# Kernel tuning notes

Hardware: AMD Instinct MI355X
Metric: run time of the kernel (lower is better)

The kernel has to match this reference:

```python
import jax, jax.numpy as jnp
import numpy as np

def setup_inputs() -> dict:
    key = jax.random.key(0)
    k1, k2 = jax.random.split(key)
    pcs1 = jax.random.normal(k1, (8, 4096, 3), dtype=jnp.float32)
    pcs2 = jax.random.normal(k2, (8, 4096, 3), dtype=jnp.float32)
    return {"pcs1": pcs1, "pcs2": pcs2}

def reference(pcs1, pcs2):
    # Pairwise squared L2 distances: [B, N, M]
    # ||a-b||^2 = ||a||^2 + ||b||^2 - 2 a.b
    sq1 = jnp.sum(pcs1 * pcs1, axis=-1)                # [B, N]
    sq2 = jnp.sum(pcs2 * pcs2, axis=-1)                # [B, M]
    inner = jnp.einsum('bnd,bmd->bnm', pcs1, pcs2)     # [B, N, M]
    d = sq1[:, :, None] + sq2[:, None, :] - 2.0 * inner
    d = jnp.maximum(d, 0.0)  # guard tiny negatives from cancellation
    dist1 = jnp.min(d, axis=2)   # [B, N] nearest in pcs2 for each point of pcs1
    dist2 = jnp.min(d, axis=1)   # [B, M] nearest in pcs1 for each point of pcs2
    loss1 = jnp.mean(jnp.sqrt(dist1))
    loss2 = jnp.mean(jnp.sqrt(dist2))
    return (loss1 + loss2) * 0.5
```

## Files before the change

### kernel.cpp

```cpp
#include <hip/hip_runtime.h>
#include <math.h>


typedef __attribute__((ext_vector_type(8)))  short bf16x8;
typedef __attribute__((ext_vector_type(16))) float f32x16;
typedef float f32x2 __attribute__((ext_vector_type(2)));

#define NPTS 4096
#define BATCH 8
#define NBLK_WORK 1024

union FragCast { uint4 u; bf16x8 v; };

__device__ __forceinline__ unsigned short f2bf(float f) {
    unsigned u = __float_as_uint(f);
    return (unsigned short)((u + 0x7FFFu + ((u >> 16) & 1u)) >> 16);
}
__device__ __forceinline__ float bf2f(unsigned short h) {
    return __uint_as_float(((unsigned)h) << 16);
}
__device__ __forceinline__ unsigned pk(unsigned short a, unsigned short b) {
    return (unsigned)a | ((unsigned)b << 16);
}

__device__ __forceinline__ void build_afrag(float x, float y, float z,
                                            uint4& a0, uint4& a1) {
    float sq  = fmaf(x, x, fmaf(y, y, z * z));
    float m2x = -2.0f * x, m2y = -2.0f * y, m2z = -2.0f * z;
    unsigned short hx = f2bf(m2x), hy = f2bf(m2y), hz = f2bf(m2z);
    unsigned short lx = f2bf(m2x - bf2f(hx));
    unsigned short ly = f2bf(m2y - bf2f(hy));
    unsigned short lz = f2bf(m2z - bf2f(hz));
    unsigned short sh = f2bf(sq);
    unsigned short sl = f2bf(sq - bf2f(sh));
    const unsigned short ONE = 0x3F80;
    a0 = make_uint4(pk(hx, hy), pk(hz, hx), pk(hy, hz), pk(lx, ly));
    a1 = make_uint4(pk(lz, lx), pk(ly, lz), pk(sh, sl), pk(ONE, ONE));
}

__device__ __forceinline__ uint4 build_bfrag(float x, float y, float z, int hf) {
    float sq = fmaf(x, x, fmaf(y, y, z * z));
    unsigned short px = f2bf(x), py = f2bf(y), pz = f2bf(z);
    unsigned short qx = f2bf(x - bf2f(px));
    unsigned short qy = f2bf(y - bf2f(py));
    unsigned short qz = f2bf(z - bf2f(pz));
    unsigned short sh = f2bf(sq);
    unsigned short sl = f2bf(sq - bf2f(sh));
    const unsigned short ONE = 0x3F80;
    return hf == 0
        ? make_uint4(pk(px, py), pk(pz, qx), pk(qy, qz), pk(px, py))
        : make_uint4(pk(pz, qx), pk(qy, qz), pk(ONE, ONE), pk(sh, sl));
}

__global__ __launch_bounds__(256, 4) void chamfer_fused(
    const float* __restrict__ pcs1, const float* __restrict__ pcs2,
    float* __restrict__ cpart, unsigned* __restrict__ counter)
{
    __shared__ uint4 afrag[2048];

    const int bid = blockIdx.x;
    const int dir = bid >> 9;
    const int b   = (bid >> 6) & 7;
    const int rq  = (bid >> 4) & 3;
    const int mg  = bid & 15;
    const int tid = threadIdx.x;

    if (bid == 0 && tid == 0) *counter = 0u;

    const float* bbase = (dir ? pcs2 : pcs1) + (size_t)b * NPTS * 3;
    const float* abase = (dir ? pcs1 : pcs2) + (size_t)b * NPTS * 3;

    const int w   = tid >> 6;
    const int l   = tid & 63;
    const int hf  = l >> 5;
    const int ln  = l & 31;

    {
        const float4* src = (const float4*)(abase + (size_t)rq * 3072);
        float4 f0 = src[3 * tid + 0];
        float4 f1 = src[3 * tid + 1];
        float4 f2 = src[3 * tid + 2];
        float xs[4] = {f0.x, f0.w, f1.z, f2.y};
        float ys[4] = {f0.y, f1.x, f1.w, f2.z};
        float zs[4] = {f0.z, f1.y, f2.x, f2.w};
        const int jt = tid >> 3;
        const int r0 = (tid & 7) * 4;
#pragma unroll
        for (int i = 0; i < 4; ++i) {
            uint4 a0, a1;
            build_afrag(xs[i], ys[i], zs[i], a0, a1);
            afrag[jt * 64 + r0 + i]      = a0;
            afrag[jt * 64 + 32 + r0 + i] = a1;
        }
    }
    __syncthreads();

    const f32x16 cz = {0.f,0.f,0.f,0.f,0.f,0.f,0.f,0.f,
                       0.f,0.f,0.f,0.f,0.f,0.f,0.f,0.f};

#pragma unroll 1
    for (int p = 0; p < 2; ++p) {
        const int mt = mg * 8 + w * 2 + p;

        FragCast bq;
        {
            const float* s = bbase + (size_t)(mt * 32 + ln) * 3;
            bq.u = build_bfrag(s[0], s[1], s[2], hf);
        }

        float acc[16];
#pragma unroll
        for (int i = 0; i < 16; ++i) acc[i] = 3.4e38f;

#pragma unroll 2
        for (int j = 0; j < 32; ++j) {
            FragCast aq;
            aq.u = afrag[j * 64 + hf * 32 + ln];
            f32x16 D = __builtin_amdgcn_mfma_f32_32x32x16_bf16(
                aq.v, bq.v, cz, 0, 0, 0);
#pragma unroll
            for (int i = 0; i < 16; ++i) acc[i] = fminf(acc[i], D[i]);
        }

        float m0 = fminf(acc[0],  acc[1]);
        float m1 = fminf(acc[2],  acc[3]);
        float m2 = fminf(acc[4],  acc[5]);
        float m3 = fminf(acc[6],  acc[7]);
        float m4 = fminf(acc[8],  acc[9]);
        float m5 = fminf(acc[10], acc[11]);
        float m6 = fminf(acc[12], acc[13]);
        float m7 = fminf(acc[14], acc[15]);
        float r  = fminf(fminf(fminf(m0, m1), fminf(m2, m3)),
                         fminf(fminf(m4, m5), fminf(m6, m7)));
        r = fminf(r, __shfl_xor(r, 32, 64));

        if (l < 32) {
            cpart[((((size_t)(dir * 8 + b) * 128 + mt) * 4 + rq) << 5) + ln] =
                fmaxf(r, 0.0f);
        }
    }
}

__global__ __launch_bounds__(256) void chamfer_red1(
    const float* __restrict__ cpart, float* __restrict__ bpart,
    unsigned* __restrict__ counter, float* __restrict__ out)
{
    __shared__ float ws4[4];
    __shared__ int islast;
    const int t  = threadIdx.x;
    const int tg = blockIdx.x * 256 + t;
    const float* p = cpart + ((size_t)(tg >> 5) << 7) + (tg & 31);
    float m = fminf(fminf(p[0], p[32]), fminf(p[64], p[96]));
    float s = sqrtf(m);
#pragma unroll
    for (int off = 1; off < 64; off <<= 1) s += __shfl_xor(s, off, 64);
    if ((t & 63) == 0) ws4[t >> 6] = s;
    __syncthreads();
    if (t == 0) {
        bpart[blockIdx.x] = ws4[0] + ws4[1] + ws4[2] + ws4[3];
        __threadfence();
        islast = (atomicAdd(counter, 1u) == 255u);
    }
    __syncthreads();
    if (islast) {
        __threadfence();
        float v = bpart[t];
#pragma unroll
        for (int off = 1; off < 64; off <<= 1) v += __shfl_xor(v, off, 64);
        if ((t & 63) == 0) ws4[t >> 6] = v;
        __syncthreads();
        if (t == 0)
            out[0] = (ws4[0] + ws4[1] + ws4[2] + ws4[3]) * (1.0f / 65536.0f);
    }
}

#define CPAIRS 1024
#define PA 16
#define RSTRIDE 68

__device__ __forceinline__ f32x2 pk_fma_lo(f32x2 c, f32x2 q, f32x2 acc) {
    f32x2 d;
    asm("v_pk_fma_f32 %0, %1, %2, %3 op_sel:[0,0,0] op_sel_hi:[0,1,1]"
        : "=v"(d) : "v"(c), "v"(q), "v"(acc));
    return d;
}
__device__ __forceinline__ f32x2 pk_fma_hi(f32x2 c, f32x2 q, f32x2 acc) {
    f32x2 d;
    asm("v_pk_fma_f32 %0, %1, %2, %3 op_sel:[1,0,0] op_sel_hi:[1,1,1]"
        : "=v"(d) : "v"(c), "v"(q), "v"(acc));
    return d;
}
__device__ __forceinline__ void vmin3(float& acc, float a, float b) {
    asm("v_min3_f32 %0, %1, %2, %3" : "=v"(acc) : "v"(acc), "v"(a), "v"(b));
}

__global__ __launch_bounds__(256, 4) void chamfer_vec(
    const float* __restrict__ pcs1, const float* __restrict__ pcs2,
    float* __restrict__ partials)
{
    __shared__ float4 lds[2 * CPAIRS];
    float4* bx = lds;
    float4* bz = lds + CPAIRS;

    const int bid = blockIdx.x;
    const int dir = bid >> 9;
    const int b   = (bid >> 6) & 7;
    const int ach = bid & 63;

    const float* A  = dir ? pcs2 : pcs1;
    const float* Bp = dir ? pcs1 : pcs2;
    const float* abase = A  + (size_t)b * NPTS * 3;
    const float* bbase = Bp + (size_t)b * NPTS * 3;

    const int tid = threadIdx.x;
    const int w   = tid >> 6;
    const int l   = tid & 63;

    const int apt = ach * 64 + w * PA;
    f32x2 cx[PA / 2], cy[PA / 2], cz2[PA / 2];
    float tmin[PA];
#pragma unroll
    for (int p2 = 0; p2 < PA / 2; ++p2) {
        const float* s = abase + (size_t)(apt + 2 * p2) * 3;
        cx[p2]  = (f32x2){-2.0f * s[0], -2.0f * s[3]};
        cy[p2]  = (f32x2){-2.0f * s[1], -2.0f * s[4]};
        cz2[p2] = (f32x2){-2.0f * s[2], -2.0f * s[5]};
        tmin[2 * p2] = 3.4e38f; tmin[2 * p2 + 1] = 3.4e38f;
    }

    for (int c = 0; c < 2; ++c) {
        if (c) __syncthreads();
#pragma unroll
        for (int i = 0; i < CPAIRS / 256; ++i) {
            int j  = i * 256 + tid;
            const float* s = bbase + (size_t)(c * CPAIRS + j) * 6;
            float x0 = s[0], y0 = s[1], z0 = s[2];
            float x1 = s[3], y1 = s[4], z1 = s[5];
            bx[j] = make_float4(x0, x1, y0, y1);
            bz[j] = make_float4(z0, z1,
                                fmaf(x0, x0, fmaf(y0, y0, z0 * z0)),
                                fmaf(x1, x1, fmaf(y1, y1, z1 * z1)));
        }
        __syncthreads();
#pragma unroll 4
        for (int t = 0; t < CPAIRS / 64; ++t) {
            float4 X = bx[t * 64 + l];
            float4 Z = bz[t * 64 + l];
            f32x2 qx = (f32x2){X.x, X.y};
            f32x2 qy = (f32x2){X.z, X.w};
            f32x2 qz = (f32x2){Z.x, Z.y};
            f32x2 qw = (f32x2){Z.z, Z.w};
#pragma unroll
            for (int p2 = 0; p2 < PA / 2; ++p2) {
                f32x2 d0 = pk_fma_lo(cz2[p2], qz, qw);
                d0 = pk_fma_lo(cy[p2], qy, d0);
                d0 = pk_fma_lo(cx[p2], qx, d0);
                vmin3(tmin[2 * p2], d0.x, d0.y);
                f32x2 d1 = pk_fma_hi(cz2[p2], qz, qw);
                d1 = pk_fma_hi(cy[p2], qy, d1);
                d1 = pk_fma_hi(cx[p2], qx, d1);
                vmin3(tmin[2 * p2 + 1], d1.x, d1.y);
            }
        }
    }

    __syncthreads();
    float* lds2 = (float*)lds;
#pragma unroll
    for (int p = 0; p < PA; ++p)
        lds2[(w * PA + p) * RSTRIDE + l] = tmin[p];
    __syncthreads();

    if (tid < 64) {
        const int g = tid;
        float m = 3.4e38f;
        const float4* row = (const float4*)&lds2[g * RSTRIDE];
#pragma unroll
        for (int i = 0; i < 16; ++i) {
            float4 v = row[i];
            m = fminf(fminf(m, fminf(v.x, v.y)), fminf(v.z, v.w));
        }
        const int ap = ach * 64 + g;
        float x = abase[ap * 3 + 0], y = abase[ap * 3 + 1], z = abase[ap * 3 + 2];
        float s = sqrtf(fmaxf(fmaf(x, x, fmaf(y, y, z * z)) + m, 0.0f));
#pragma unroll
        for (int off = 1; off < 64; off <<= 1) s += __shfl_xor(s, off, 64);
        if (g == 0) partials[bid] = s;
    }
}

__global__ __launch_bounds__(256) void chamfer_final(
    const float* __restrict__ partials, int n, float scale,
    float* __restrict__ out)
{
    __shared__ float ws4[4];
    const int t = threadIdx.x;
    float v = 0.0f;
    for (int i = t; i < n; i += 256) v += partials[i];
#pragma unroll
    for (int off = 1; off < 64; off <<= 1) v += __shfl_xor(v, off, 64);
    if ((t & 63) == 0) ws4[t >> 6] = v;
    __syncthreads();
    if (t == 0)
        out[0] = (ws4[0] + ws4[1] + ws4[2] + ws4[3]) * scale;
}

extern "C" void kernel_launch(void* const* d_in, const int* in_sizes, int n_in,
                              void* d_out, int out_size, void* d_ws, size_t ws_size,
                              hipStream_t stream) {
    const float* pcs1 = (const float*)d_in[0];
    const float* pcs2 = (const float*)d_in[1];
    float* out = (float*)d_out;

    const size_t MB = 1048576;
    const size_t need = MB + 4096;

    if (ws_size >= need) {
        char* w = (char*)d_ws;
        float*    cpart   = (float*)(w);
        float*    bpart   = (float*)(w + MB);
        unsigned* counter = (unsigned*)(w + MB + 1024);

        chamfer_fused<<<dim3(NBLK_WORK), dim3(256), 0, stream>>>(
            pcs1, pcs2, cpart, counter);
        chamfer_red1 <<<dim3(256), dim3(256), 0, stream>>>(
            cpart, bpart, counter, out);
    } else {
        float* partials = (float*)d_ws;
        chamfer_vec  <<<dim3(1024), dim3(256), 0, stream>>>(pcs1, pcs2, partials);
        chamfer_final<<<dim3(1),    dim3(256), 0, stream>>>(
            partials, 1024, 1.0f / 65536.0f, out);
    }
}
```

Baseline: 24.61 us.

## Fuse chamfer compute and reduction into one cooperative kernel with grid sync

```diff
diff --git a/kernel.cpp b/kernel.cpp
--- a/kernel.cpp
+++ b/kernel.cpp
@@ -1,5 +1,8 @@
 #include <hip/hip_runtime.h>
+#include <hip/hip_cooperative_groups.h>
 #include <math.h>
+
+namespace cg = cooperative_groups;
 
 
 typedef __attribute__((ext_vector_type(8)))  short bf16x8;
@@ -8,7 +11,6 @@
 
 #define NPTS 4096
 #define BATCH 8
-#define NBLK_WORK 1024
 
 union FragCast { uint4 u; bf16x8 v; };
 
@@ -52,20 +54,19 @@
         : make_uint4(pk(pz, qx), pk(qy, qz), pk(ONE, ONE), pk(sh, sl));
 }
 
-__global__ __launch_bounds__(256, 4) void chamfer_fused(
+__global__ __launch_bounds__(512, 4) void chamfer_coop(
     const float* __restrict__ pcs1, const float* __restrict__ pcs2,
-    float* __restrict__ cpart, unsigned* __restrict__ counter)
+    float* __restrict__ bpart, float* __restrict__ out)
 {
     __shared__ uint4 afrag[2048];
+    __shared__ float ldsmin[256];
+    __shared__ float wavesum[8];
 
     const int bid = blockIdx.x;
-    const int dir = bid >> 9;
-    const int b   = (bid >> 6) & 7;
-    const int rq  = (bid >> 4) & 3;
-    const int mg  = bid & 15;
+    const int dir = bid >> 8;
+    const int b   = (bid >> 5) & 7;
+    const int mgr = bid & 31;
     const int tid = threadIdx.x;
-
-    if (bid == 0 && tid == 0) *counter = 0u;
 
     const float* bbase = (dir ? pcs2 : pcs1) + (size_t)b * NPTS * 3;
     const float* abase = (dir ? pcs1 : pcs2) + (size_t)b * NPTS * 3;
@@ -74,54 +75,59 @@
     const int l   = tid & 63;
     const int hf  = l >> 5;
     const int ln  = l & 31;
-
+    const int mt  = mgr * 4 + (w & 3);
+    const int rh  = w >> 2;
+
+    FragCast bq;
     {
-        const float4* src = (const float4*)(abase + (size_t)rq * 3072);
-        float4 f0 = src[3 * tid + 0];
-        float4 f1 = src[3 * tid + 1];
-        float4 f2 = src[3 * tid + 2];
-        float xs[4] = {f0.x, f0.w, f1.z, f2.y};
-        float ys[4] = {f0.y, f1.x, f1.w, f2.z};
-        float zs[4] = {f0.z, f1.y, f2.x, f2.w};
-        const int jt = tid >> 3;
-        const int r0 = (tid & 7) * 4;
-#pragma unroll
-        for (int i = 0; i < 4; ++i) {
-            uint4 a0, a1;
-            build_afrag(xs[i], ys[i], zs[i], a0, a1);
-            afrag[jt * 64 + r0 + i]      = a0;
-            afrag[jt * 64 + 32 + r0 + i] = a1;
-        }
-    }
-    __syncthreads();
+        const float* s = bbase + (size_t)(mt * 32 + ln) * 3;
+        bq.u = build_bfrag(s[0], s[1], s[2], hf);
+    }
 
     const f32x16 cz = {0.f,0.f,0.f,0.f,0.f,0.f,0.f,0.f,
                        0.f,0.f,0.f,0.f,0.f,0.f,0.f,0.f};
+    float acc[16];
+#pragma unroll
+    for (int i = 0; i < 16; ++i) acc[i] = 3.4e38f;
 
 #pragma unroll 1
-    for (int p = 0; p < 2; ++p) {
-        const int mt = mg * 8 + w * 2 + p;
-
-        FragCast bq;
-        {
-            const float* s = bbase + (size_t)(mt * 32 + ln) * 3;
-            bq.u = build_bfrag(s[0], s[1], s[2], hf);
-        }
-
-        float acc[16];
-#pragma unroll
-        for (int i = 0; i < 16; ++i) acc[i] = 3.4e38f;
+    for (int ph = 0; ph < 4; ++ph) {
+        if (ph) __syncthreads();
+        if (tid < 256) {
+            const int g = tid >> 7;
+            const int t = tid & 127;
+            const float4* src =
+                (const float4*)(abase + ((size_t)g * 2048 + ph * 512) * 3);
+            float4 f0 = src[3 * t + 0];
+            float4 f1 = src[3 * t + 1];
+            float4 f2 = src[3 * t + 2];
+            float xs[4] = {f0.x, f0.w, f1.z, f2.y};
+            float ys[4] = {f0.y, f1.x, f1.w, f2.z};
+            float zs[4] = {f0.z, f1.y, f2.x, f2.w};
+            const int jt = t >> 3;
+            const int r0 = (t & 7) * 4;
+#pragma unroll
+            for (int i = 0; i < 4; ++i) {
+                uint4 a0, a1;
+                build_afrag(xs[i], ys[i], zs[i], a0, a1);
+                afrag[g * 1024 + jt * 64 + r0 + i]      = a0;
+                afrag[g * 1024 + jt * 64 + 32 + r0 + i] = a1;
+            }
+        }
+        __syncthreads();
 
 #pragma unroll 2
-        for (int j = 0; j < 32; ++j) {
+        for (int j = 0; j < 16; ++j) {
             FragCast aq;
-            aq.u = afrag[j * 64 + hf * 32 + ln];
+            aq.u = afrag[rh * 1024 + j * 64 + hf * 32 + ln];
             f32x16 D = __builtin_amdgcn_mfma_f32_32x32x16_bf16(
                 aq.v, bq.v, cz, 0, 0, 0);
 #pragma unroll
             for (int i = 0; i < 16; ++i) acc[i] = fminf(acc[i], D[i]);
         }
-
+    }
+
+    {
         float m0 = fminf(acc[0],  acc[1]);
         float m1 = fminf(acc[2],  acc[3]);
         float m2 = fminf(acc[4],  acc[5]);
@@ -133,6 +139,120 @@
         float r  = fminf(fminf(fminf(m0, m1), fminf(m2, m3)),
                          fminf(fminf(m4, m5), fminf(m6, m7)));
         r = fminf(r, __shfl_xor(r, 32, 64));
+        if (l < 32) ldsmin[w * 32 + ln] = r;
+    }
+    __syncthreads();
+
+    float s = 0.0f;
+    if (tid < 128) {
+        const int wl = tid >> 5;
+        const int c  = tid & 31;
+        float m = fminf(ldsmin[wl * 32 + c], ldsmin[(wl + 4) * 32 + c]);
+        s = sqrtf(fmaxf(m, 0.0f));
+    }
+#pragma unroll
+    for (int off = 1; off < 64; off <<= 1) s += __shfl_xor(s, off, 64);
+    if ((tid & 63) == 0) wavesum[tid >> 6] = s;
+    __syncthreads();
+    if (tid == 0) bpart[bid] = wavesum[0] + wavesum[1];
+
+    cg::this_grid().sync();
+
+    if (bid == 0) {
+        float v = bpart[tid];
+#pragma unroll
+        for (int off = 1; off < 64; off <<= 1) v += __shfl_xor(v, off, 64);
+        if ((tid & 63) == 0) wavesum[tid >> 6] = v;
+        __syncthreads();
+        if (tid == 0) {
+            float tot = wavesum[0] + wavesum[1] + wavesum[2] + wavesum[3]
+                      + wavesum[4] + wavesum[5] + wavesum[6] + wavesum[7];
+            out[0] = tot * (1.0f / 65536.0f);
+        }
+    }
+}
+
+__global__ __launch_bounds__(256, 4) void chamfer_fused(
+    const float* __restrict__ pcs1, const float* __restrict__ pcs2,
+    float* __restrict__ cpart, unsigned* __restrict__ counter)
+{
+    __shared__ uint4 afrag[2048];
+
+    const int bid = blockIdx.x;
+    const int dir = bid >> 9;
+    const int b   = (bid >> 6) & 7;
+    const int rq  = (bid >> 4) & 3;
+    const int mg  = bid & 15;
+    const int tid = threadIdx.x;
+
+    if (bid == 0 && tid == 0) *counter = 0u;
+
+    const float* bbase = (dir ? pcs2 : pcs1) + (size_t)b * NPTS * 3;
+    const float* abase = (dir ? pcs1 : pcs2) + (size_t)b * NPTS * 3;
+
+    const int w   = tid >> 6;
+    const int l   = tid & 63;
+    const int hf  = l >> 5;
+    const int ln  = l & 31;
+
+    {
+        const float4* src = (const float4*)(abase + (size_t)rq * 3072);
+        float4 f0 = src[3 * tid + 0];
+        float4 f1 = src[3 * tid + 1];
+        float4 f2 = src[3 * tid + 2];
+        float xs[4] = {f0.x, f0.w, f1.z, f2.y};
+        float ys[4] = {f0.y, f1.x, f1.w, f2.z};
+        float zs[4] = {f0.z, f1.y, f2.x, f2.w};
+        const int jt = tid >> 3;
+        const int r0 = (tid & 7) * 4;
+#pragma unroll
+        for (int i = 0; i < 4; ++i) {
+            uint4 a0, a1;
+            build_afrag(xs[i], ys[i], zs[i], a0, a1);
+            afrag[jt * 64 + r0 + i]      = a0;
+            afrag[jt * 64 + 32 + r0 + i] = a1;
+        }
+    }
+    __syncthreads();
+
+    const f32x16 cz = {0.f,0.f,0.f,0.f,0.f,0.f,0.f,0.f,
+                       0.f,0.f,0.f,0.f,0.f,0.f,0.f,0.f};
+
+#pragma unroll 1
+    for (int p = 0; p < 2; ++p) {
+        const int mt = mg * 8 + w * 2 + p;
+
+        FragCast bq;
+        {
+            const float* s = bbase + (size_t)(mt * 32 + ln) * 3;
+            bq.u = build_bfrag(s[0], s[1], s[2], hf);
+        }
+
+        float acc[16];
+#pragma unroll
+        for (int i = 0; i < 16; ++i) acc[i] = 3.4e38f;
+
+#pragma unroll 2
+        for (int j = 0; j < 32; ++j) {
+            FragCast aq;
+            aq.u = afrag[j * 64 + hf * 32 + ln];
+            f32x16 D = __builtin_amdgcn_mfma_f32_32x32x16_bf16(
+                aq.v, bq.v, cz, 0, 0, 0);
+#pragma unroll
+            for (int i = 0; i < 16; ++i) acc[i] = fminf(acc[i], D[i]);
+        }
+
+        float m0 = fminf(acc[0],  acc[1]);
+        float m1 = fminf(acc[2],  acc[3]);
+        float m2 = fminf(acc[4],  acc[5]);
+        float m3 = fminf(acc[6],  acc[7]);
+        float m4 = fminf(acc[8],  acc[9]);
+        float m5 = fminf(acc[10], acc[11]);
+        float m6 = fminf(acc[12], acc[13]);
+        float m7 = fminf(acc[14], acc[15]);
+        float r  = fminf(fminf(fminf(m0, m1), fminf(m2, m3)),
+                         fminf(fminf(m4, m5), fminf(m6, m7)));
+        r = fminf(r, __shfl_xor(r, 32, 64));
 
         if (l < 32) {
             cpart[((((size_t)(dir * 8 + b) * 128 + mt) * 4 + rq) << 5) + ln] =
@@ -313,15 +433,23 @@
     float* out = (float*)d_out;
 
     const size_t MB = 1048576;
-    const size_t need = MB + 4096;
-
-    if (ws_size >= need) {
+
+    if (ws_size >= 4096) {
+        float* bpart = (float*)d_ws;
+        void* args[4] = {(void*)&pcs1, (void*)&pcs2, (void*)&bpart, (void*)&out};
+        hipError_t err = hipLaunchCooperativeKernel(
+            (const void*)chamfer_coop, dim3(512), dim3(512), args, 0, stream);
+        if (err == hipSuccess) return;
+        (void)hipGetLastError();
+    }
+
+    if (ws_size >= MB + 4096) {
         char* w = (char*)d_ws;
         float*    cpart   = (float*)(w);
         float*    bpart   = (float*)(w + MB);
         unsigned* counter = (unsigned*)(w + MB + 1024);
 
-        chamfer_fused<<<dim3(NBLK_WORK), dim3(256), 0, stream>>>(
+        chamfer_fused<<<dim3(1024), dim3(256), 0, stream>>>(
             pcs1, pcs2, cpart, counter);
         chamfer_red1 <<<dim3(256), dim3(256), 0, stream>>>(
             cpart, bpart, counter, out);
```

New measurement: 69.56 us. +182.6%, slower.
